# Kernel tuning notes

Measured on AMD Instinct MI355X. Metric: run time of the kernel, lower is better.

## Reference

```python
import jax, jax.numpy as jnp
import numpy as np

# MPO / tensor-train setup for a 768 -> 3072 linear (BERT-base FFN)
IN_SHAPE = (3, 4, 4, 4, 4)    # prod = 768
OUT_SHAPE = (4, 4, 8, 6, 4)   # prod = 3072
# untruncated TT ranks: r_k = min(prod_{j<=k} i_j*o_j, prod_{j>k} i_j*o_j)
RANKS = (1, 12, 192, 384, 16, 1)
CORE_SCALE = 0.05  # keep reconstructed matrix well-conditioned in fp32


def setup_inputs() -> dict:
    key = jax.random.key(0)
    ks = jax.random.split(key, 7)
    x = jax.random.normal(ks[0], (8, 4096, 768), dtype=jnp.float32)
    cores = {}
    for k in range(5):
        shape = (RANKS[k], IN_SHAPE[k], OUT_SHAPE[k], RANKS[k + 1])
        cores[f"core{k}"] = jax.random.normal(ks[1 + k], shape, dtype=jnp.float32) * CORE_SCALE
    bias = jax.random.normal(ks[6], (3072,), dtype=jnp.float32)
    return {"x": x, **cores, "bias": bias}


def _mpo2matrix(cores):
    """Contract TT cores [r_{k-1}, i_k, o_k, r_k] into dense [prod(i), prod(o)]."""
    t = cores[0][0]  # [i0, o0, r1]
    for c in cores[1:]:
        # t: [I, O, r], c: [r, i, o, q] -> [I*i, O*o, q]
        t = jnp.einsum('IOr,rioq->IiOoq', t, c)
        I, i, O, o, q = t.shape
        t = t.reshape(I * i, O * o, q)
    return t[:, :, 0]  # [768, 3072]


def reference(x, core0, core1, core2, core3, core4, bias):
    # F.linear(res, mpo2matrix(tensor_set), bias): y = x_flat @ M + b
    M = _mpo2matrix([core0, core1, core2, core3, core4])  # [in, out] = [768, 3072]
    x_flat = x.reshape(-1, x.shape[-1])                    # [B*S, 768]
    y = x_flat @ M + bias                                  # [B*S, 3072]
    return y.reshape(x.shape[:-1] + (M.shape[1],))
```

## Files before the change

kernel.cpp:

```cpp
#include <hip/hip_runtime.h>
#include <hip/hip_bf16.h>
#include <stdint.h>
#include <stddef.h>


typedef __attribute__((ext_vector_type(8))) short short8;
typedef __attribute__((ext_vector_type(4))) float floatx4;

#define DEVINL __device__ __forceinline__

DEVINL void gload_lds16(const void* g, void* l) {
  __builtin_amdgcn_global_load_lds(
      (const __attribute__((address_space(1))) unsigned int*)g,
      (__attribute__((address_space(3))) unsigned int*)l, 16, 0, 0);
}

DEVINL unsigned short f2bf(float f) {
  unsigned int u = __float_as_uint(f);
  u = u + 0x7fffu + ((u >> 16) & 1u);
  return (unsigned short)(u >> 16);
}

__global__ __launch_bounds__(256) void cast_x_kernel(
    const float4* __restrict__ x4, ushort4* __restrict__ xb4, int n4) {
  int i = blockIdx.x * blockDim.x + threadIdx.x;
  if (i >= n4) return;
  float4 v = x4[i];
  ushort4 o;
  o.x = f2bf(v.x); o.y = f2bf(v.y); o.z = f2bf(v.z); o.w = f2bf(v.w);
  xb4[i] = o;
}

__global__ __launch_bounds__(256) void tt_gemm(
    const float* __restrict__ A, const float* __restrict__ B,
    float* __restrict__ C, unsigned short* __restrict__ Ct,
    int M, int K, int N, int Odim, int idim, int odim, int qdim,
    int final_bf16_transpose) {
  __shared__ float sA[64][17];
  __shared__ float sB[16][68];
  const int tid = threadIdx.x;
  const int tx = tid & 15, ty = tid >> 4;
  const int bm = blockIdx.y, bn = blockIdx.x;
  float acc[4][4] = {};
  const int arow = tid >> 2;
  const int acol = (tid & 3) * 4;
  const int brow = tid >> 4;
  const int bcol = (tid & 15) * 4;

  for (int k0 = 0; k0 < K; k0 += 16) {
    {
      int r = bm * 64 + arow;
#pragma unroll
      for (int j = 0; j < 4; j++) {
        int k = k0 + acol + j;
        sA[arow][acol + j] = (r < M && k < K) ? A[(size_t)r * K + k] : 0.f;
      }
      int kb = k0 + brow;
#pragma unroll
      for (int j = 0; j < 4; j++) {
        int c = bn * 64 + bcol + j;
        sB[brow][bcol + j] = (kb < K && c < N) ? B[(size_t)kb * N + c] : 0.f;
      }
    }
    __syncthreads();
#pragma unroll 4
    for (int kb = 0; kb < 16; kb++) {
      float ra[4], rb[4];
#pragma unroll
      for (int r = 0; r < 4; r++) ra[r] = sA[ty * 4 + r][kb];
#pragma unroll
      for (int c = 0; c < 4; c++) rb[c] = sB[kb][tx * 4 + c];
#pragma unroll
      for (int r = 0; r < 4; r++)
#pragma unroll
        for (int c = 0; c < 4; c++) acc[r][c] += ra[r] * rb[c];
    }
    __syncthreads();
  }

  const int oq = odim * qdim;
#pragma unroll
  for (int r = 0; r < 4; r++) {
    int row = bm * 64 + ty * 4 + r;
    if (row >= M) continue;
    int I = row / Odim, O = row - I * Odim;
#pragma unroll
    for (int c = 0; c < 4; c++) {
      int col = bn * 64 + tx * 4 + c;
      if (col >= N) continue;
      int i = col / oq; int rem = col - i * oq;
      int o = rem / qdim; int q = rem - o * qdim;
      size_t dst = ((((size_t)I * idim + i) * Odim + O) * (size_t)odim + o) * qdim + q;
      if (final_bf16_transpose) {
        size_t in_ = dst / 3072, out_ = dst - in_ * 3072;
        Ct[out_ * 768 + in_] = f2bf(acc[r][c]);
      } else {
        C[dst] = acc[r][c];
      }
    }
  }
}

__global__ __launch_bounds__(256) void mpo_gemm(
    const unsigned short* __restrict__ Xb,
    const unsigned short* __restrict__ Mt,
    const float* __restrict__ bias,
    float* __restrict__ out) {
  __shared__ __align__(16) unsigned short sA[128 * 64];
  __shared__ __align__(16) unsigned short sB[128 * 64];
  const int tid = threadIdx.x;
  const int lane = tid & 63;
  const int wave = tid >> 6;
  const int bm = blockIdx.y, bn = blockIdx.x;

  const int is_b = wave >> 1;
  const int half = wave & 1;
  const unsigned short* gbase = is_b ? Mt : Xb;
  unsigned short* lds_base = is_b ? sB : sA;
  const int tile_row0 = (is_b ? bn : bm) * 128 + half * 64;
  const int lrow = lane >> 3;
  const int segg = (lane & 7) ^ lrow;
  const unsigned short* gptr[8];
#pragma unroll
  for (int j = 0; j < 8; j++)
    gptr[j] = gbase + (size_t)(tile_row0 + j * 8 + lrow) * 768 + segg * 8;

  const int wm = wave & 1, wn = wave >> 1;
  const int row15 = lane & 15;
  const int kg = lane >> 4;

  floatx4 acc[4][4];
#pragma unroll
  for (int mi = 0; mi < 4; mi++)
#pragma unroll
    for (int ni = 0; ni < 4; ni++) acc[mi][ni] = (floatx4){0.f, 0.f, 0.f, 0.f};

  for (int k0 = 0; k0 < 768; k0 += 64) {
    __syncthreads();
#pragma unroll
    for (int j = 0; j < 8; j++) {
      unsigned short* l = lds_base + (half * 64 + j * 8) * 64;
      gload_lds16(gptr[j] + k0, l);
    }
    __syncthreads();

#pragma unroll
    for (int kk = 0; kk < 2; kk++) {
      short8 af[4], bfv[4];
#pragma unroll
      for (int mi = 0; mi < 4; mi++) {
        int row = wm * 64 + mi * 16 + row15;
        int sp = (kk * 4 + kg) ^ (row & 7);
        af[mi] = *(const short8*)(sA + row * 64 + sp * 8);
      }
#pragma unroll
      for (int ni = 0; ni < 4; ni++) {
        int row = wn * 64 + ni * 16 + row15;
        int sp = (kk * 4 + kg) ^ (row & 7);
        bfv[ni] = *(const short8*)(sB + row * 64 + sp * 8);
      }
#pragma unroll
      for (int mi = 0; mi < 4; mi++)
#pragma unroll
        for (int ni = 0; ni < 4; ni++)
          acc[mi][ni] = __builtin_amdgcn_mfma_f32_16x16x32_bf16(
              af[mi], bfv[ni], acc[mi][ni], 0, 0, 0);
    }
  }

  const int crow = (lane >> 4) * 4;
  const int ccol = lane & 15;
#pragma unroll
  for (int ni = 0; ni < 4; ni++) {
    int col = bn * 128 + wn * 64 + ni * 16 + ccol;
    float bv = bias[col];
#pragma unroll
    for (int mi = 0; mi < 4; mi++) {
      int row0 = bm * 128 + wm * 64 + mi * 16 + crow;
      floatx4 v = acc[mi][ni];
#pragma unroll
      for (int r = 0; r < 4; r++)
        out[(size_t)(row0 + r) * 3072 + col] = v[r] + bv;
    }
  }
}

#define OFF_T2 0u
#define OFF_T3 147456u
#define OFF_T4 9584640u
#define OFF_MT 19021824u
#define OFF_XB 23740416u

extern "C" void kernel_launch(void* const* d_in, const int* in_sizes, int n_in,
                              void* d_out, int out_size, void* d_ws, size_t ws_size,
                              hipStream_t stream) {
  const float* x  = (const float*)d_in[0];
  const float* c0 = (const float*)d_in[1];
  const float* c1 = (const float*)d_in[2];
  const float* c2 = (const float*)d_in[3];
  const float* c3 = (const float*)d_in[4];
  const float* c4 = (const float*)d_in[5];
  const float* bias = (const float*)d_in[6];
  float* out = (float*)d_out;
  char* ws = (char*)d_ws;

  float* t2 = (float*)(ws + OFF_T2);
  float* t3 = (float*)(ws + OFF_T3);
  float* t4 = (float*)(ws + OFF_T4);
  unsigned short* Mt = (unsigned short*)(ws + OFF_MT);
  unsigned short* xb = (unsigned short*)(ws + OFF_XB);

  cast_x_kernel<<<dim3(24576), dim3(256), 0, stream>>>(
      (const float4*)x, (ushort4*)xb, 6291456);

  tt_gemm<<<dim3(48, 1), dim3(256), 0, stream>>>(
      c0, c1, t2, nullptr, 12, 12, 3072, 4, 4, 4, 192, 0);
  tt_gemm<<<dim3(192, 3), dim3(256), 0, stream>>>(
      t2, c2, t3, nullptr, 192, 192, 12288, 16, 4, 8, 384, 0);
  tt_gemm<<<dim3(6, 96), dim3(256), 0, stream>>>(
      t3, c3, t4, nullptr, 6144, 384, 384, 128, 4, 6, 16, 0);
  tt_gemm<<<dim3(1, 2304), dim3(256), 0, stream>>>(
      t4, c4, nullptr, Mt, 147456, 16, 16, 768, 4, 4, 1, 1);

  mpo_gemm<<<dim3(24, 256), dim3(256), 0, stream>>>(xb, Mt, bias, out);
}
```

Baseline: 820.0 us.

## Merge last two TT cores, add register-tiled TT GEMMs, swizzle MPO block order

Contracts core3 and core4 into one 384x384 matrix up front, so the last two tensor-train steps collapse into a single GEMM. That GEMM writes the transposed bf16 weight directly, removing the large t4 intermediate and the skinny K=16 GEMM. New templated fp32 GEMMs use 64x128 tiles, 4x8 per-thread outputs, float4 loads, register prefetch of the next K slice and vectorized stores. The main bf16 GEMM also remaps block indices so neighbouring blocks share weight tiles in L2. The added reassociation slightly changes fp32 rounding order.

```diff
diff --git a/kernel.cpp b/kernel.cpp
--- a/kernel.cpp
+++ b/kernel.cpp
@@ -101,6 +101,129 @@
   }
 }
 
+__global__ __launch_bounds__(256) void b34_build(
+    const float* __restrict__ c3, const float* __restrict__ c4,
+    float* __restrict__ B34) {
+  int e = blockIdx.x * 256 + threadIdx.x;
+  int r3 = e / 384; int c = e - r3 * 384;
+  int i34 = c / 24, o34 = c - i34 * 24;
+  int i3 = i34 >> 2, i4 = i34 & 3;
+  int o3 = o34 >> 2, o4 = o34 & 3;
+  const float* p3 = c3 + (((size_t)r3 * 4 + i3) * 6 + o3) * 16;
+  const float* p4 = c4 + i4 * 4 + o4;
+  float s = 0.f;
+#pragma unroll
+  for (int r4 = 0; r4 < 16; r4++) s += p3[r4] * p4[r4 * 16];
+  B34[e] = s;
+}
+
+template <int STEP>
+__global__ __launch_bounds__(256) void tt_fast(
+    const float* __restrict__ A, const float* __restrict__ B,
+    float* __restrict__ C, unsigned short* __restrict__ Ct) {
+  constexpr int K  = (STEP == 2) ? 192 : 384;
+  constexpr int NN = (STEP == 2) ? 12288 : 384;
+  constexpr int NT = K / 32;
+  __shared__ __align__(16) float sAt[32][68];
+  __shared__ __align__(16) float sB[32][144];
+  const int tid = threadIdx.x;
+  const int tx = tid & 15, ty = tid >> 4;
+  const int bm = blockIdx.y, bn = blockIdx.x;
+
+  const int arow = tid >> 3;
+  const int akq  = (tid & 7) * 4;
+  const int brow = tid >> 5;
+  const int bq   = tid & 31;
+  const float* gA = A + (size_t)(bm * 64 + arow) * K + akq;
+  const float* gB = B + (size_t)brow * NN + bn * 128 + bq * 4;
+  const int bso = bq * 4 + ((bq >> 3) << 2);
+  const int rb_off = tx * 8 + ((tx >> 2) << 2);
+
+  float4 a0 = *(const float4*)(gA);
+  float4 a1 = *(const float4*)(gA + (size_t)32 * K);
+  float4 b0 = *(const float4*)(gB);
+  float4 b1 = *(const float4*)(gB + (size_t)8 * NN);
+  float4 b2 = *(const float4*)(gB + (size_t)16 * NN);
+  float4 b3 = *(const float4*)(gB + (size_t)24 * NN);
+
+  float acc[4][8];
+#pragma unroll
+  for (int r = 0; r < 4; r++)
+#pragma unroll
+    for (int c = 0; c < 8; c++) acc[r][c] = 0.f;
+
+  for (int t = 0; t < NT; t++) {
+    __syncthreads();
+    sAt[akq + 0][arow]      = a0.x;
+    sAt[akq + 1][arow]      = a0.y;
+    sAt[akq + 2][arow]      = a0.z;
+    sAt[akq + 3][arow]      = a0.w;
+    sAt[akq + 0][arow + 32] = a1.x;
+    sAt[akq + 1][arow + 32] = a1.y;
+    sAt[akq + 2][arow + 32] = a1.z;
+    sAt[akq + 3][arow + 32] = a1.w;
+    *(float4*)&sB[brow][bso]      = b0;
+    *(float4*)&sB[brow + 8][bso]  = b1;
+    *(float4*)&sB[brow + 16][bso] = b2;
+    *(float4*)&sB[brow + 24][bso] = b3;
+    __syncthreads();
+    if (t + 1 < NT) {
+      const float* pA = gA + (t + 1) * 32;
+      a0 = *(const float4*)(pA);
+      a1 = *(const float4*)(pA + (size_t)32 * K);
+      const float* pB = gB + (size_t)(t + 1) * 32 * NN;
+      b0 = *(const float4*)(pB);
+      b1 = *(const float4*)(pB + (size_t)8 * NN);
+      b2 = *(const float4*)(pB + (size_t)16 * NN);
+      b3 = *(const float4*)(pB + (size_t)24 * NN);
+    }
+#pragma unroll 8
+    for (int k = 0; k < 32; k++) {
+      const float4 ra  = *(const float4*)&sAt[k][ty * 4];
+      const float4 rb0 = *(const float4*)&sB[k][rb_off];
+      const float4 rb1 = *(const float4*)&sB[k][rb_off + 4];
+      const float av[4] = {ra.x, ra.y, ra.z, ra.w};
+      const float bv[8] = {rb0.x, rb0.y, rb0.z, rb0.w,
+                           rb1.x, rb1.y, rb1.z, rb1.w};
+#pragma unroll
+      for (int r = 0; r < 4; r++)
+#pragma unroll
+        for (int c = 0; c < 8; c++) acc[r][c] += av[r] * bv[c];
+    }
+  }
+
+  if constexpr (STEP == 2) {
+    const int colbase = bn * 128 + tx * 8;
+    const int g = colbase / 384;
+    const int r3 = colbase - g * 384;
+    const int i2 = g >> 3, o2 = g & 7;
+#pragma unroll
+    for (int r = 0; r < 4; r++) {
+      int m = bm * 64 + ty * 4 + r;
+      int I = m >> 4, O = m & 15;
+      size_t drow = (size_t)((I * 4 + i2) * 128 + O * 8 + o2);
+      float4 v0 = {acc[r][0], acc[r][1], acc[r][2], acc[r][3]};
+      float4 v1 = {acc[r][4], acc[r][5], acc[r][6], acc[r][7]};
+      *(float4*)(C + drow * 384 + r3)     = v0;
+      *(float4*)(C + drow * 384 + r3 + 4) = v1;
+    }
+  } else {
+    const int colbase = bn * 128 + tx * 8;
+#pragma unroll
+    for (int r = 0; r < 4; r++) {
+      int m2 = bm * 64 + ty * 4 + r;
+      int Iin = m2 >> 7, Oout = m2 & 127;
+#pragma unroll
+      for (int c = 0; c < 8; c++) {
+        int col = colbase + c;
+        int i34 = col / 24;
+        int o34 = col - i34 * 24;
+        Ct[(size_t)(Oout * 24 + o34) * 768 + Iin * 16 + i34] = f2bf(acc[r][c]);
+      }
+    }
+  }
+}
+
 __global__ __launch_bounds__(256) void mpo_gemm(
     const unsigned short* __restrict__ Xb,
     const unsigned short* __restrict__ Mt,
@@ -111,7 +234,10 @@
   const int tid = threadIdx.x;
   const int lane = tid & 63;
   const int wave = tid >> 6;
-  const int bm = blockIdx.y, bn = blockIdx.x;
+  const int lin = blockIdx.y * 24 + blockIdx.x;
+  const int nid = (lin & 7) * 768 + (lin >> 3);
+  const int bn = nid % 24;
+  const int bm = nid / 24;
 
   const int is_b = wave >> 1;
   const int half = wave & 1;
@@ -185,11 +311,11 @@
   }
 }
 
-#define OFF_T2 0u
-#define OFF_T3 147456u
-#define OFF_T4 9584640u
-#define OFF_MT 19021824u
-#define OFF_XB 23740416u
+#define OFF_T2  0u
+#define OFF_T3  147456u
+#define OFF_B34 9584640u
+#define OFF_MT  10174464u
+#define OFF_XB  14893056u
 
 extern "C" void kernel_launch(void* const* d_in, const int* in_sizes, int n_in,
                               void* d_out, int out_size, void* d_ws, size_t ws_size,
@@ -206,7 +332,7 @@
 
   float* t2 = (float*)(ws + OFF_T2);
   float* t3 = (float*)(ws + OFF_T3);
-  float* t4 = (float*)(ws + OFF_T4);
+  float* B34 = (float*)(ws + OFF_B34);
   unsigned short* Mt = (unsigned short*)(ws + OFF_MT);
   unsigned short* xb = (unsigned short*)(ws + OFF_XB);
 
@@ -215,12 +341,12 @@
 
   tt_gemm<<<dim3(48, 1), dim3(256), 0, stream>>>(
       c0, c1, t2, nullptr, 12, 12, 3072, 4, 4, 4, 192, 0);
-  tt_gemm<<<dim3(192, 3), dim3(256), 0, stream>>>(
-      t2, c2, t3, nullptr, 192, 192, 12288, 16, 4, 8, 384, 0);
-  tt_gemm<<<dim3(6, 96), dim3(256), 0, stream>>>(
-      t3, c3, t4, nullptr, 6144, 384, 384, 128, 4, 6, 16, 0);
-  tt_gemm<<<dim3(1, 2304), dim3(256), 0, stream>>>(
-      t4, c4, nullptr, Mt, 147456, 16, 16, 768, 4, 4, 1, 1);
+
+  b34_build<<<dim3(576), dim3(256), 0, stream>>>(c3, c4, B34);
+
+  tt_fast<2><<<dim3(96, 3), dim3(256), 0, stream>>>(t2, c2, t3, nullptr);
+
+  tt_fast<3><<<dim3(3, 96), dim3(256), 0, stream>>>(t3, B34, nullptr, Mt);
 
   mpo_gemm<<<dim3(24, 256), dim3(256), 0, stream>>>(xb, Mt, bias, out);
 }
```

Measured after the change: 749.9 us. 8.5% less time.
